# Kernel tuning notes

Hardware: AMD Instinct MI355X
Metric: run time of the kernel (lower is better)

## Reference

```python
import jax, jax.numpy as jnp
import numpy as np

B = 131072          # points on manifold
A = 16              # n_anchors
SDIM = 512          # substrate.n (spatial dim); ambient dim = SDIM + 1
ALPHA = 0.1         # attraction coefficient
EPS = 1e-7


def _proj(p):
    # Project onto hyperboloid: recompute time coord from spatial part.
    sp = p[..., 1:]
    t = jnp.sqrt(1.0 + jnp.sum(sp * sp, axis=-1, keepdims=True))
    return jnp.concatenate([t, sp], axis=-1)


def _linner(x, y):
    # Lorentz inner product <x,y>_L = -x0*y0 + sum_i xi*yi
    return -x[..., 0] * y[..., 0] + jnp.sum(x[..., 1:] * y[..., 1:], axis=-1)


def setup_inputs() -> dict:
    key = jax.random.key(0)
    k1, k2 = jax.random.split(key)
    x_sp = jax.random.normal(k1, (B, SDIM), dtype=jnp.float32)
    x = _proj(jnp.concatenate([jnp.zeros((B, 1), jnp.float32), x_sp], axis=-1))
    a_sp = jax.random.normal(k2, (A, SDIM), dtype=jnp.float32) * 0.01
    anchors = _proj(jnp.concatenate([jnp.zeros((A, 1), jnp.float32), a_sp], axis=-1))
    return {"x": x, "anchors": anchors}


def reference(x, anchors):
    af = _proj(anchors)                                   # [A, D]
    D = af.shape[-1]
    metric = jnp.concatenate([-jnp.ones((1,), x.dtype), jnp.ones((D - 1,), x.dtype)])
    # pairwise -<x,a>_L  -> [B, A]
    theta_all = -jnp.einsum('bd,ad->ba', x * metric, af)
    dists = jnp.arccosh(jnp.clip(theta_all, 1.0 + EPS, None))
    idx = jnp.argmin(dists, axis=1)                       # nearest anchor per point
    y = af[idx]                                           # [B, D]
    # log_map_x(y) = acosh(theta)/sqrt(theta^2-1) * (y - theta*x)
    theta = jnp.clip(-_linner(x, y), 1.0 + EPS, None)[:, None]
    direction = (jnp.arccosh(theta) / jnp.sqrt(theta * theta - 1.0)) * (y - theta * x)
    v = ALPHA * direction                                 # tangent vector
    # exp_map_x(v) = cosh(||v||_L) x + sinh(||v||_L)/||v||_L * v
    vn = jnp.sqrt(jnp.clip(_linner(v, v), EPS, None))[:, None]
    return jnp.cosh(vn) * x + (jnp.sinh(vn) / vn) * v
```

## Files before the change

### kernel.cpp

```cpp
#include <hip/hip_runtime.h>

#define B_ROWS 131072
#define NA 16
#define DD 513
#define ALPHA 0.1f
#define EPSV 1e-7f

__global__ __launch_bounds__(256, 2)
void hfield_kernel(const float* __restrict__ x,
                   const float* __restrict__ anc,
                   float* __restrict__ out) {
    __shared__ float lds_af[NA * DD];
    __shared__ __attribute__((aligned(16))) float redbuf[4][64 * 20];

    const int tid  = threadIdx.x;
    const int lane = tid & 63;
    const int wid  = tid >> 6;
    const int gw   = blockIdx.x * 4 + wid;
    const int TW   = gridDim.x * 4;

    for (int i = tid; i < NA * DD; i += 256) lds_af[i] = anc[i];

    float Areg[NA][8];
#pragma unroll
    for (int a = 0; a < NA; ++a) {
#pragma unroll
        for (int j = 0; j < 8; ++j)
            Areg[a][j] = anc[a * DD + 1 + lane + 64 * j];
    }

    float* wb = redbuf[wid];
    const int g     = lane >> 4;
    const int amine = lane & 15;

    float af0;
    {
        float q[NA];
#pragma unroll
        for (int a = 0; a < NA; ++a) {
            float s = 0.f;
#pragma unroll
            for (int j = 0; j < 8; ++j) s = fmaf(Areg[a][j], Areg[a][j], s);
            q[a] = s;
        }
#pragma unroll
        for (int t4 = 0; t4 < 4; ++t4)
            *reinterpret_cast<float4*>(&wb[lane * 20 + 4 * t4]) =
                make_float4(q[4 * t4], q[4 * t4 + 1], q[4 * t4 + 2], q[4 * t4 + 3]);
        asm volatile("s_waitcnt lgkmcnt(0)" ::: "memory");
        float t = 0.f;
#pragma unroll
        for (int k = 0; k < 16; ++k) t += wb[(g + 4 * k) * 20 + amine];
        t += __shfl_xor(t, 16);
        t += __shfl_xor(t, 32);
        af0 = sqrtf(1.0f + t);
    }

    __syncthreads();

    const float thmin = 1.0f + 1e-7f;

    int row = gw;
    float xn[8], x0n = 0.f;
    if (row < B_ROWS) {
        const float* rp = x + (size_t)row * DD;
        x0n = rp[0];
#pragma unroll
        for (int j = 0; j < 8; ++j) xn[j] = rp[1 + lane + 64 * j];
    }

    for (; row < B_ROWS; row += TW) {
        float xc[8];
        const float x0 = x0n;
#pragma unroll
        for (int j = 0; j < 8; ++j) xc[j] = xn[j];

        const int nrow = row + TW;
        if (nrow < B_ROWS) {
            const float* rp = x + (size_t)nrow * DD;
            x0n = rp[0];
#pragma unroll
            for (int j = 0; j < 8; ++j) xn[j] = rp[1 + lane + 64 * j];
        }

        float q[NA];
#pragma unroll
        for (int a = 0; a < NA; ++a) {
            float s = 0.f;
#pragma unroll
            for (int j = 0; j < 8; ++j) s = fmaf(xc[j], Areg[a][j], s);
            q[a] = s;
        }

#pragma unroll
        for (int t4 = 0; t4 < 4; ++t4)
            *reinterpret_cast<float4*>(&wb[lane * 20 + 4 * t4]) =
                make_float4(q[4 * t4], q[4 * t4 + 1], q[4 * t4 + 2], q[4 * t4 + 3]);
        asm volatile("s_waitcnt lgkmcnt(0)" ::: "memory");
        float t = 0.f;
#pragma unroll
        for (int k = 0; k < 16; ++k) t += wb[(g + 4 * k) * 20 + amine];
        t += __shfl_xor(t, 16);
        t += __shfl_xor(t, 32);

        float tc = fmaxf(fmaf(x0, af0, -t), thmin);
        int   bi = amine;

#pragma unroll
        for (int m = 1; m <= 8; m <<= 1) {
            float vo = __shfl_xor(tc, m);
            int   io = __shfl_xor(bi, m);
            bool take = (vo < tc) || (vo == tc && io < bi);
            tc = take ? vo : tc;
            bi = take ? io : bi;
        }

        float s2   = tc * tc - 1.0f;
        float rr   = sqrtf(s2);
        float ach  = logf(tc + rr);
        float coef = ach / rr;
        float vn   = sqrtf(fmaxf(ALPHA * ALPHA * ach * ach, EPSV));
        float e    = expf(vn);
        float ei   = 1.0f / e;
        float ch   = 0.5f * (e + ei);
        float sh   = 0.5f * (e - ei);
        float c2   = ALPHA * coef * (sh / vn);
        float c1   = fmaf(-c2, tc, ch);

        float* op = out + (size_t)row * DD;
        const float* yp = lds_af + bi * DD + 1 + lane;
#pragma unroll
        for (int j = 0; j < 8; ++j) {
            float y = yp[64 * j];
            __builtin_nontemporal_store(fmaf(c2, y, c1 * xc[j]), &op[1 + lane + 64 * j]);
        }
        float y0   = __shfl(af0, bi);
        float out0 = fmaf(c2, y0, c1 * x0);
        if (lane == 0) __builtin_nontemporal_store(out0, &op[0]);
    }
}

extern "C" void kernel_launch(void* const* d_in, const int* in_sizes, int n_in,
                              void* d_out, int out_size, void* d_ws, size_t ws_size,
                              hipStream_t stream) {
    const float* x   = (const float*)d_in[0];
    const float* anc = (const float*)d_in[1];
    float* out       = (float*)d_out;
    hipLaunchKernelGGL(hfield_kernel, dim3(1024), dim3(256), 0, stream, x, anc, out);
}
```

Baseline: 116.2 us.

## Use fp16 packed dot products with anchors in LDS and shuffle-based reduction

Anchors are packed into fp16 pairs in LDS, and the point–anchor inner products are computed with fdot2 instructions instead of fp32 FMAs held in registers. A transpose-style shuffle reduction replaces the LDS scratch reduction. Each wave now handles a fixed block of 16 contiguous rows with a two-row-deep prefetch and 8-contiguous-float loads per lane. The grid is doubled and occupancy is raised. The output y is also rebuilt from fp16 anchors and fast log/exp intrinsics are used, which reduces accuracy and may change argmin ties.

After: 143.9 us. 1.24x slower.

```diff
diff --git a/kernel.cpp b/kernel.cpp
--- a/kernel.cpp
+++ b/kernel.cpp
@@ -1,142 +1,179 @@
 #include <hip/hip_runtime.h>
 
-#define B_ROWS 131072
 #define NA 16
 #define DD 513
 #define ALPHA 0.1f
 #define EPSV 1e-7f
+#define RPW 16
+#define GRID 2048
 
-__global__ __launch_bounds__(256, 2)
+typedef __fp16 h2 __attribute__((ext_vector_type(2)));
+typedef unsigned int u32;
+
+union H2U { h2 h; u32 u; };
+
+static __device__ __forceinline__ u32 pkrtz(float lo, float hi) {
+    H2U t; t.h = __builtin_amdgcn_cvt_pkrtz(lo, hi); return t.u;
+}
+static __device__ __forceinline__ h2 asH2(u32 w) { H2U t; t.u = w; return t.h; }
+
+static __device__ __forceinline__ float fdot2(u32 a, u32 b, float c) {
+#if __has_builtin(__builtin_amdgcn_fdot2)
+    return __builtin_amdgcn_fdot2(asH2(a), asH2(b), c, false);
+#else
+    h2 ha = asH2(a), hb = asH2(b);
+    c = fmaf((float)ha.x, (float)hb.x, c);
+    return fmaf((float)ha.y, (float)hb.y, c);
+#endif
+}
+
+struct __attribute__((packed, aligned(4))) F4 { float a, b, c, d; };
+
+#define RSTEP(m, half)                                              \
+    _Pragma("unroll")                                               \
+    for (int i = 0; i < half; ++i) {                                \
+        const bool up = (lane & m) != 0;                            \
+        float snd = up ? v[i] : v[half + i];                        \
+        float kp  = up ? v[half + i] : v[i];                        \
+        v[i] = kp + __shfl_xor(snd, m);                             \
+    }
+
+static __device__ __forceinline__ float reduce16(float v[16], int lane) {
+    RSTEP(1, 8)
+    RSTEP(2, 4)
+    RSTEP(4, 2)
+    RSTEP(8, 1)
+    float S = v[0];
+    S += __shfl_xor(S, 16);
+    S += __shfl_xor(S, 32);
+    return S;
+}
+
+__global__ __launch_bounds__(256, 4)
 void hfield_kernel(const float* __restrict__ x,
                    const float* __restrict__ anc,
                    float* __restrict__ out) {
-    __shared__ float lds_af[NA * DD];
-    __shared__ __attribute__((aligned(16))) float redbuf[4][64 * 20];
+    __shared__ u32 ah[NA][256];
 
-    const int tid  = threadIdx.x;
-    const int lane = tid & 63;
-    const int wid  = tid >> 6;
-    const int gw   = blockIdx.x * 4 + wid;
-    const int TW   = gridDim.x * 4;
+    const int tid = threadIdx.x, lane = tid & 63, wid = tid >> 6;
 
-    for (int i = tid; i < NA * DD; i += 256) lds_af[i] = anc[i];
+    for (int i = tid; i < NA * 256; i += 256) {
+        const int a = i >> 8, w = i & 255;
+        ah[a][w] = pkrtz(anc[a * DD + 1 + 2 * w], anc[a * DD + 2 + 2 * w]);
+    }
+    __syncthreads();
 
-    float Areg[NA][8];
-#pragma unroll
-    for (int a = 0; a < NA; ++a) {
-#pragma unroll
-        for (int j = 0; j < 8; ++j)
-            Areg[a][j] = anc[a * DD + 1 + lane + 64 * j];
-    }
-
-    float* wb = redbuf[wid];
-    const int g     = lane >> 4;
-    const int amine = lane & 15;
+    const int aidx = ((lane & 1) << 3) | (((lane >> 1) & 1) << 2) |
+                     (((lane >> 2) & 1) << 1) | ((lane >> 3) & 1);
 
     float af0;
     {
-        float q[NA];
+        float v[16];
 #pragma unroll
         for (int a = 0; a < NA; ++a) {
-            float s = 0.f;
-#pragma unroll
-            for (int j = 0; j < 8; ++j) s = fmaf(Areg[a][j], Areg[a][j], s);
-            q[a] = s;
+            const uint4 w = *reinterpret_cast<const uint4*>(&ah[a][4 * lane]);
+            float s = fdot2(w.x, w.x, 0.f);
+            s = fdot2(w.y, w.y, s);
+            s = fdot2(w.z, w.z, s);
+            v[a] = fdot2(w.w, w.w, s);
         }
-#pragma unroll
-        for (int t4 = 0; t4 < 4; ++t4)
-            *reinterpret_cast<float4*>(&wb[lane * 20 + 4 * t4]) =
-                make_float4(q[4 * t4], q[4 * t4 + 1], q[4 * t4 + 2], q[4 * t4 + 3]);
-        asm volatile("s_waitcnt lgkmcnt(0)" ::: "memory");
-        float t = 0.f;
-#pragma unroll
-        for (int k = 0; k < 16; ++k) t += wb[(g + 4 * k) * 20 + amine];
-        t += __shfl_xor(t, 16);
-        t += __shfl_xor(t, 32);
-        af0 = sqrtf(1.0f + t);
+        af0 = sqrtf(1.0f + reduce16(v, lane));
     }
 
-    __syncthreads();
+    const int gw = blockIdx.x * 4 + wid;
+    const float* rbase = x + (size_t)gw * RPW * DD;
+    float*       obase = out + (size_t)gw * RPW * DD;
 
-    const float thmin = 1.0f + 1e-7f;
-
-    int row = gw;
-    float xn[8], x0n = 0.f;
-    if (row < B_ROWS) {
-        const float* rp = x + (size_t)row * DD;
-        x0n = rp[0];
-#pragma unroll
-        for (int j = 0; j < 8; ++j) xn[j] = rp[1 + lane + 64 * j];
+    float xa[8], xb[8];
+    float x0a, x0b;
+    {
+        const float* p = rbase + 1 + 8 * lane;
+        F4 lo = *(const F4*)p, hi = *(const F4*)(p + 4);
+        xa[0] = lo.a; xa[1] = lo.b; xa[2] = lo.c; xa[3] = lo.d;
+        xa[4] = hi.a; xa[5] = hi.b; xa[6] = hi.c; xa[7] = hi.d;
+        x0a = rbase[0];
+        const float* q = rbase + DD + 1 + 8 * lane;
+        F4 lo2 = *(const F4*)q, hi2 = *(const F4*)(q + 4);
+        xb[0] = lo2.a; xb[1] = lo2.b; xb[2] = lo2.c; xb[3] = lo2.d;
+        xb[4] = hi2.a; xb[5] = hi2.b; xb[6] = hi2.c; xb[7] = hi2.d;
+        x0b = rbase[DD];
     }
 
-    for (; row < B_ROWS; row += TW) {
-        float xc[8];
-        const float x0 = x0n;
-#pragma unroll
-        for (int j = 0; j < 8; ++j) xc[j] = xn[j];
-
-        const int nrow = row + TW;
-        if (nrow < B_ROWS) {
-            const float* rp = x + (size_t)nrow * DD;
-            x0n = rp[0];
-#pragma unroll
-            for (int j = 0; j < 8; ++j) xn[j] = rp[1 + lane + 64 * j];
+#pragma unroll 1
+    for (int it = 0; it < RPW; ++it) {
+        float xn[8] = {0, 0, 0, 0, 0, 0, 0, 0};
+        float x0n = 0.f;
+        if (it + 2 < RPW) {
+            const float* p = rbase + (size_t)(it + 2) * DD;
+            F4 lo = *(const F4*)(p + 1 + 8 * lane);
+            F4 hi = *(const F4*)(p + 5 + 8 * lane);
+            xn[0] = lo.a; xn[1] = lo.b; xn[2] = lo.c; xn[3] = lo.d;
+            xn[4] = hi.a; xn[5] = hi.b; xn[6] = hi.c; xn[7] = hi.d;
+            x0n = p[0];
         }
 
-        float q[NA];
+        const u32 xp0 = pkrtz(xa[0], xa[1]);
+        const u32 xp1 = pkrtz(xa[2], xa[3]);
+        const u32 xp2 = pkrtz(xa[4], xa[5]);
+        const u32 xp3 = pkrtz(xa[6], xa[7]);
+
+        float v[16];
 #pragma unroll
         for (int a = 0; a < NA; ++a) {
-            float s = 0.f;
-#pragma unroll
-            for (int j = 0; j < 8; ++j) s = fmaf(xc[j], Areg[a][j], s);
-            q[a] = s;
+            const uint4 w = *reinterpret_cast<const uint4*>(&ah[a][4 * lane]);
+            float s = fdot2(w.x, xp0, 0.f);
+            s = fdot2(w.y, xp1, s);
+            s = fdot2(w.z, xp2, s);
+            v[a] = fdot2(w.w, xp3, s);
         }
+        const float S = reduce16(v, lane);
 
-#pragma unroll
-        for (int t4 = 0; t4 < 4; ++t4)
-            *reinterpret_cast<float4*>(&wb[lane * 20 + 4 * t4]) =
-                make_float4(q[4 * t4], q[4 * t4 + 1], q[4 * t4 + 2], q[4 * t4 + 3]);
-        asm volatile("s_waitcnt lgkmcnt(0)" ::: "memory");
-        float t = 0.f;
-#pragma unroll
-        for (int k = 0; k < 16; ++k) t += wb[(g + 4 * k) * 20 + amine];
-        t += __shfl_xor(t, 16);
-        t += __shfl_xor(t, 32);
-
-        float tc = fmaxf(fmaf(x0, af0, -t), thmin);
-        int   bi = amine;
-
+        float tc = fmaxf(fmaf(x0a, af0, -S), 1.0f + 1e-7f);
+        int idx = aidx;
 #pragma unroll
         for (int m = 1; m <= 8; m <<= 1) {
             float vo = __shfl_xor(tc, m);
-            int   io = __shfl_xor(bi, m);
-            bool take = (vo < tc) || (vo == tc && io < bi);
-            tc = take ? vo : tc;
-            bi = take ? io : bi;
+            int   io = __shfl_xor(idx, m);
+            bool take = (vo < tc) || (vo == tc && io < idx);
+            tc  = take ? vo : tc;
+            idx = take ? io : idx;
         }
+        const int bi = __builtin_amdgcn_readfirstlane(idx);
 
-        float s2   = tc * tc - 1.0f;
-        float rr   = sqrtf(s2);
-        float ach  = logf(tc + rr);
-        float coef = ach / rr;
-        float vn   = sqrtf(fmaxf(ALPHA * ALPHA * ach * ach, EPSV));
-        float e    = expf(vn);
-        float ei   = 1.0f / e;
-        float ch   = 0.5f * (e + ei);
-        float sh   = 0.5f * (e - ei);
-        float c2   = ALPHA * coef * (sh / vn);
-        float c1   = fmaf(-c2, tc, ch);
+        const float s2   = tc * tc - 1.0f;
+        const float rr   = sqrtf(s2);
+        const float ach  = __logf(tc + rr);
+        const float coef = ach / rr;
+        const float vn   = sqrtf(fmaxf(ALPHA * ALPHA * ach * ach, EPSV));
+        const float e    = __expf(vn);
+        const float ei   = 1.0f / e;
+        const float ch   = 0.5f * (e + ei);
+        const float sh   = 0.5f * (e - ei);
+        const float c2   = ALPHA * coef * (sh / vn);
+        const float c1   = fmaf(-c2, tc, ch);
 
-        float* op = out + (size_t)row * DD;
-        const float* yp = lds_af + bi * DD + 1 + lane;
+        const uint4 wy = *reinterpret_cast<const uint4*>(&ah[bi][4 * lane]);
+        float yv[8];
+        { h2 t = asH2(wy.x); yv[0] = (float)t.x; yv[1] = (float)t.y; }
+        { h2 t = asH2(wy.y); yv[2] = (float)t.x; yv[3] = (float)t.y; }
+        { h2 t = asH2(wy.z); yv[4] = (float)t.x; yv[5] = (float)t.y; }
+        { h2 t = asH2(wy.w); yv[6] = (float)t.x; yv[7] = (float)t.y; }
+
+        float* op = obase + (size_t)it * DD;
+        float* sp = op + 1 + 8 * lane;
 #pragma unroll
-        for (int j = 0; j < 8; ++j) {
-            float y = yp[64 * j];
-            __builtin_nontemporal_store(fmaf(c2, y, c1 * xc[j]), &op[1 + lane + 64 * j]);
-        }
-        float y0   = __shfl(af0, bi);
-        float out0 = fmaf(c2, y0, c1 * x0);
-        if (lane == 0) __builtin_nontemporal_store(out0, &op[0]);
+        for (int j = 0; j < 8; ++j)
+            __builtin_nontemporal_store(fmaf(c2, yv[j], c1 * xa[j]), &sp[j]);
+
+        const int lsrc = ((bi >> 3) & 1) | (((bi >> 2) & 1) << 1) |
+                         (((bi >> 1) & 1) << 2) | ((bi & 1) << 3);
+        const float y0 = __shfl(af0, lsrc);
+        if (lane == 0)
+            __builtin_nontemporal_store(fmaf(c2, y0, c1 * x0a), op);
+
+#pragma unroll
+        for (int j = 0; j < 8; ++j) { xa[j] = xb[j]; xb[j] = xn[j]; }
+        x0a = x0b; x0b = x0n;
     }
 }
 
@@ -146,5 +183,5 @@
     const float* x   = (const float*)d_in[0];
     const float* anc = (const float*)d_in[1];
     float* out       = (float*)d_out;
-    hipLaunchKernelGGL(hfield_kernel, dim3(1024), dim3(256), 0, stream, x, anc, out);
+    hipLaunchKernelGGL(hfield_kernel, dim3(GRID), dim3(256), 0, stream, x, anc, out);
 }
```
